# Kernel optimization log

Hardware: AMD Instinct MI355X
Metric: run time of the kernel (lower is better)

## Reference

```python
import jax, jax.numpy as jnp
import numpy as np

B, T, D = 16, 4096, 1024
UNITS = 1024


def setup_inputs() -> dict:
    key = jax.random.key(0)
    ks = jax.random.split(key, 8)
    s_in = 1.0 / np.sqrt(D)
    s_u = 1.0 / np.sqrt(UNITS)
    return {
        "hidden_state": jax.random.normal(ks[0], (B, D), jnp.float32),
        "encoder_output": jax.random.normal(ks[1], (B, T, D), jnp.float32),
        "W1": jax.random.normal(ks[2], (D, UNITS), jnp.float32) * s_in,
        "b1": jnp.zeros((UNITS,), jnp.float32),
        "W2": jax.random.normal(ks[3], (D, UNITS), jnp.float32) * s_in,
        "b2": jnp.zeros((UNITS,), jnp.float32),
        "V": jax.random.normal(ks[4], (UNITS, 1), jnp.float32) * s_u,
        "bv": jnp.zeros((1,), jnp.float32),
    }


def reference(hidden_state, encoder_output, W1, b1, W2, b2, V, bv):
    # Bahdanau additive attention: score = V(tanh(W1(h) + W2(enc)))
    h_proj = hidden_state @ W1 + b1                      # [B, U]
    e_proj = jnp.einsum("btd,du->btu", encoder_output, W2) + b2  # [B, T, U]
    feat = jnp.tanh(h_proj[:, None, :] + e_proj)          # [B, T, U]
    score = feat @ V + bv                                 # [B, T, 1]
    attention_weights = jax.nn.softmax(score, axis=1)     # [B, T, 1]
    context_vector = jnp.sum(attention_weights * encoder_output, axis=1)  # [B, D]
    return context_vector, attention_weights
```

## Files before the change

kernel.cpp:

```cpp
#include <hip/hip_runtime.h>
#include <hip/hip_bf16.h>
#include <math.h>

#define B_ 16
#define T_ 4096
#define D_ 1024
#define U_ 1024
#define M_ (B_*T_)

typedef __attribute__((ext_vector_type(8))) short short8;
typedef __attribute__((ext_vector_type(4))) short short4v;
typedef __attribute__((ext_vector_type(4))) float float4v;

static __device__ __forceinline__ short f2bf(float f) {
    unsigned u = __builtin_bit_cast(unsigned, f);
    u += 0x7FFFu + ((u >> 16) & 1u);
    return (short)(u >> 16);
}
static __device__ __forceinline__ float bf2f(short s) {
    unsigned u = ((unsigned)(unsigned short)s) << 16;
    return __builtin_bit_cast(float, u);
}
static __device__ __forceinline__ float fast_tanh(float x) {
    float c = fminf(fmaxf(2.f * x, -30.f), 30.f);
    float t = __expf(c);
    return __fdividef(t - 1.f, t + 1.f);
}

#define GLLDS(GP, LP) __builtin_amdgcn_global_load_lds( \
    (const __attribute__((address_space(1))) void*)(GP), \
    (__attribute__((address_space(3))) void*)(LP), 16, 0, 0)

__global__ void hb_kernel(const float* __restrict__ h, const float* __restrict__ W1,
                          const float* __restrict__ b1, const float* __restrict__ b2,
                          float* __restrict__ hbp) {
    int x = blockIdx.x;
    int kc = x >> 6;
    int gid = (x & 63) * 256 + threadIdx.x;
    int b = gid >> 10, u = gid & 1023;
    const float* hr = h + b * D_ + kc * 256;
    const float* w = W1 + (size_t)(kc * 256) * U_ + u;
    float s0 = 0.f, s1 = 0.f, s2 = 0.f, s3 = 0.f;
    for (int k = 0; k < 256; k += 4) {
        s0 += hr[k+0] * w[(size_t)(k+0) * U_];
        s1 += hr[k+1] * w[(size_t)(k+1) * U_];
        s2 += hr[k+2] * w[(size_t)(k+2) * U_];
        s3 += hr[k+3] * w[(size_t)(k+3) * U_];
    }
    float s = ((s0 + s1) + (s2 + s3));
    if (kc == 0) s += b1[u] + b2[u];
    hbp[kc * 16384 + gid] = s;
}

__global__ void convert_enc(const float* __restrict__ enc, short* __restrict__ encbf) {
    size_t g = (size_t)blockIdx.x * 256 + threadIdx.x;
    const float4v* p = (const float4v*)(enc + g * 16);
    float4v f0 = p[0], f1 = p[1], f2 = p[2], f3 = p[3];
    short8 a, b;
    a[0]=f2bf(f0[0]); a[1]=f2bf(f0[1]); a[2]=f2bf(f0[2]); a[3]=f2bf(f0[3]);
    a[4]=f2bf(f1[0]); a[5]=f2bf(f1[1]); a[6]=f2bf(f1[2]); a[7]=f2bf(f1[3]);
    b[0]=f2bf(f2[0]); b[1]=f2bf(f2[1]); b[2]=f2bf(f2[2]); b[3]=f2bf(f2[3]);
    b[4]=f2bf(f3[0]); b[5]=f2bf(f3[1]); b[6]=f2bf(f3[2]); b[7]=f2bf(f3[3]);
    short8* q = (short8*)(encbf + g * 16);
    q[0] = a; q[1] = b;
}

__global__ void convert_w2t(const float* __restrict__ W2, short* __restrict__ W2T) {
    __shared__ short t[64][65];
    int k0 = (blockIdx.x >> 4) * 64, u0 = (blockIdx.x & 15) * 64;
    int tx = threadIdx.x & 63, ty = threadIdx.x >> 6;
    #pragma unroll
    for (int r = 0; r < 16; ++r) {
        int kk = ty * 16 + r;
        t[kk][tx] = f2bf(W2[(size_t)(k0 + kk) * U_ + u0 + tx]);
    }
    __syncthreads();
    #pragma unroll
    for (int r = 0; r < 16; ++r) {
        int uu = ty * 16 + r;
        W2T[(size_t)(u0 + uu) * D_ + k0 + tx] = t[tx][uu];
    }
}

__global__ __launch_bounds__(256) void gemm_score_bf16(
    const short* __restrict__ Abf,
    const short* __restrict__ W2T,
    const float* __restrict__ hbp,
    const float* __restrict__ V,
    float* __restrict__ scorepart)
{
    __shared__ __align__(16) short As[128 * 32];
    __shared__ __align__(16) short Bs[128 * 32];
    __shared__ float sbuf[2][128];

    const int tid = threadIdx.x;
    const int g = blockIdx.x;
    const int c = g & 7, q = g >> 3;
    const int ntile = q & 7;
    const int mtile = (q >> 3) * 8 + c;
    const int row0 = mtile * 128, n0 = ntile * 128;
    const int bidx = row0 >> 12;

    const int lane = tid & 63, wv = tid >> 6;
    const int wm = wv >> 1, wn = wv & 1;
    const int lm = lane & 15, quad = lane >> 4;
    const int arow = tid >> 2, akq = (tid & 3) * 8;

    float4v acc[4][4] = {};

    for (int K0 = 0; K0 < D_; K0 += 32) {
        GLLDS(Abf + (size_t)(row0 + arow) * D_ + K0 + akq,       As + tid * 8);
        GLLDS(Abf + (size_t)(row0 + 64 + arow) * D_ + K0 + akq,  As + 2048 + tid * 8);
        GLLDS(W2T + (size_t)(n0 + arow) * D_ + K0 + akq,         Bs + tid * 8);
        GLLDS(W2T + (size_t)(n0 + 64 + arow) * D_ + K0 + akq,    Bs + 2048 + tid * 8);
        __syncthreads();
        short8 af[4], bfr[4];
        #pragma unroll
        for (int mi = 0; mi < 4; ++mi)
            af[mi] = *(const short8*)&As[(wm * 64 + mi * 16 + lm) * 32 + quad * 8];
        #pragma unroll
        for (int ni = 0; ni < 4; ++ni)
            bfr[ni] = *(const short8*)&Bs[(wn * 64 + ni * 16 + lm) * 32 + quad * 8];
        #pragma unroll
        for (int mi = 0; mi < 4; ++mi)
            #pragma unroll
            for (int ni = 0; ni < 4; ++ni)
                acc[mi][ni] = __builtin_amdgcn_mfma_f32_16x16x32_bf16(
                    af[mi], bfr[ni], acc[mi][ni], 0, 0, 0);
        __syncthreads();
    }

    float hbv[4], Vv[4];
    #pragma unroll
    for (int ni = 0; ni < 4; ++ni) {
        int U = n0 + wn * 64 + ni * 16 + lm;
        int o = bidx * U_ + U;
        hbv[ni] = hbp[o] + hbp[16384 + o] + hbp[32768 + o] + hbp[49152 + o];
        Vv[ni]  = V[U];
    }
    #pragma unroll
    for (int mi = 0; mi < 4; ++mi) {
        #pragma unroll
        for (int r = 0; r < 4; ++r) {
            float s = 0.f;
            #pragma unroll
            for (int ni = 0; ni < 4; ++ni)
                s += fast_tanh(acc[mi][ni][r] + hbv[ni]) * Vv[ni];
            #pragma unroll
            for (int off = 1; off < 16; off <<= 1)
                s += __shfl_xor(s, off, 64);
            if (lm == 0)
                sbuf[wn][wm * 64 + mi * 16 + quad * 4 + r] = s;
        }
    }
    __syncthreads();
    if (tid < 128)
        scorepart[(size_t)ntile * M_ + row0 + tid] = sbuf[0][tid] + sbuf[1][tid];
}

__global__ __launch_bounds__(1024) void softmax_kernel(
        const float* __restrict__ scorepart,
        const float* __restrict__ bv,
        float* __restrict__ out_attn) {
    __shared__ float sm[T_];
    __shared__ float redm[16];
    __shared__ float reds[16];
    int b = blockIdx.x, tid = threadIdx.x;
    int wv = tid >> 6;
    float bvv = bv[0];
    float lmax = -1e30f;
    #pragma unroll
    for (int i = 0; i < 4; ++i) {
        int t = tid + i * 1024;
        float s = bvv;
        #pragma unroll
        for (int p = 0; p < 8; ++p) s += scorepart[(size_t)p * M_ + b * T_ + t];
        sm[t] = s;
        lmax = fmaxf(lmax, s);
    }
    #pragma unroll
    for (int off = 1; off < 64; off <<= 1) lmax = fmaxf(lmax, __shfl_xor(lmax, off, 64));
    if ((tid & 63) == 0) redm[wv] = lmax;
    __syncthreads();
    float m = redm[0];
    #pragma unroll
    for (int j = 1; j < 16; ++j) m = fmaxf(m, redm[j]);
    float lsum = 0.f;
    #pragma unroll
    for (int i = 0; i < 4; ++i) {
        int t = tid + i * 1024;
        float e = __expf(sm[t] - m);
        sm[t] = e;
        lsum += e;
    }
    #pragma unroll
    for (int off = 1; off < 64; off <<= 1) lsum += __shfl_xor(lsum, off, 64);
    if ((tid & 63) == 0) reds[wv] = lsum;
    __syncthreads();
    float tot = 0.f;
    #pragma unroll
    for (int j = 0; j < 16; ++j) tot += reds[j];
    float rinv = 1.f / tot;
    #pragma unroll
    for (int i = 0; i < 4; ++i) {
        int t = tid + i * 1024;
        out_attn[b * T_ + t] = sm[t] * rinv;
    }
}

__global__ void ctx_part_bf(const short* __restrict__ encbf,
                            const float* __restrict__ attn,
                            float* __restrict__ part) {
    __shared__ float wsm[128];
    int x = blockIdx.x;
    int b = x & 15, tc = x >> 4;
    int tid = threadIdx.x;
    if (tid < 128) wsm[tid] = attn[b * T_ + tc * 128 + tid];
    __syncthreads();
    const short* e0 = encbf + (size_t)(b * T_ + tc * 128) * D_ + tid * 4;
    float4v acc = {};
    for (int t = 0; t < 128; ++t) {
        short4v v = *(const short4v*)(e0 + (size_t)t * D_);
        float w = wsm[t];
        acc[0] += w * bf2f(v[0]);
        acc[1] += w * bf2f(v[1]);
        acc[2] += w * bf2f(v[2]);
        acc[3] += w * bf2f(v[3]);
    }
    *(float4v*)(part + (size_t)x * 1024 + tid * 4) = acc;
}

__global__ void ctx_reduce_kernel(const float* __restrict__ part, float* __restrict__ ctx) {
    int gid = blockIdx.x * 256 + threadIdx.x;
    int b = gid >> 10, d = gid & 1023;
    float s = 0.f;
    #pragma unroll
    for (int tc = 0; tc < 32; ++tc) s += part[(size_t)(tc * 16 + b) * 1024 + d];
    ctx[gid] = s;
}

extern "C" void kernel_launch(void* const* d_in, const int* in_sizes, int n_in,
                              void* d_out, int out_size, void* d_ws, size_t ws_size,
                              hipStream_t stream) {
    const float* h   = (const float*)d_in[0];
    const float* enc = (const float*)d_in[1];
    const float* W1  = (const float*)d_in[2];
    const float* b1  = (const float*)d_in[3];
    const float* W2  = (const float*)d_in[4];
    const float* b2  = (const float*)d_in[5];
    const float* V   = (const float*)d_in[6];
    const float* bv  = (const float*)d_in[7];
    float* out = (float*)d_out;
    float* ws  = (float*)d_ws;

    float* hbp       = ws;
    float* scorepart = ws + 65536;
    float* ctxpart   = scorepart;
    short* W2T   = (short*)(ws + 65536 + 524288);
    short* encbf = (short*)((char*)W2T + (size_t)U_ * D_ * 2);

    hb_kernel<<<256, 256, 0, stream>>>(h, W1, b1, b2, hbp);
    convert_enc<<<16384, 256, 0, stream>>>(enc, encbf);
    convert_w2t<<<256, 256, 0, stream>>>(W2, W2T);
    gemm_score_bf16<<<4096, 256, 0, stream>>>(encbf, W2T, hbp, V, scorepart);
    softmax_kernel<<<16, 1024, 0, stream>>>(scorepart, bv, out + 16384);
    ctx_part_bf<<<512, 256, 0, stream>>>(encbf, out + 16384, ctxpart);
    ctx_reduce_kernel<<<64, 256, 0, stream>>>(ctxpart, out);
}
```

Before: 606.3 us.

## Rewrite score GEMM as 256x256 tile, 8-wave, double-buffered phased pipeline

The bf16 score GEMM moves from 128x128 tiles with 4 waves and a single-buffered K=32 loop to 256x256 tiles with 8 waves, K=64 steps, XOR-swizzled LDS and double buffering. Each K step is split into four MFMA phases. Global-to-LDS loads for later steps are interleaved between the phases, with explicit barriers, s_setprio and vmcnt waits. The larger tile halves the number of N-tile partial scores, so softmax now sums 4 partials instead of 8. The cost is 128KB of LDS and heavy register use, which limits occupancy, and the hand-managed waitcnt and barrier logic is fragile.

```diff
diff --git a/kernel.cpp b/kernel.cpp
--- a/kernel.cpp
+++ b/kernel.cpp
@@ -82,54 +82,136 @@
     }
 }
 
-__global__ __launch_bounds__(256) void gemm_score_bf16(
+__global__ __launch_bounds__(512, 2) void gemm_score_8ph(
     const short* __restrict__ Abf,
     const short* __restrict__ W2T,
     const float* __restrict__ hbp,
     const float* __restrict__ V,
     float* __restrict__ scorepart)
 {
-    __shared__ __align__(16) short As[128 * 32];
-    __shared__ __align__(16) short Bs[128 * 32];
-    __shared__ float sbuf[2][128];
+    __shared__ __align__(16) short lds[65536];
 
     const int tid = threadIdx.x;
     const int g = blockIdx.x;
     const int c = g & 7, q = g >> 3;
-    const int ntile = q & 7;
-    const int mtile = (q >> 3) * 8 + c;
-    const int row0 = mtile * 128, n0 = ntile * 128;
+    const int ntile = q & 3;
+    const int mtile = (q >> 2) * 8 + c;
+    const int row0 = mtile * 256, n0 = ntile * 256;
     const int bidx = row0 >> 12;
 
-    const int lane = tid & 63, wv = tid >> 6;
-    const int wm = wv >> 1, wn = wv & 1;
+    const int lane = tid & 63;
+    const int wv = tid >> 6;
+    const int wm = wv >> 2, wn = wv & 3;
     const int lm = lane & 15, quad = lane >> 4;
-    const int arow = tid >> 2, akq = (tid & 3) * 8;
-
-    float4v acc[4][4] = {};
-
-    for (int K0 = 0; K0 < D_; K0 += 32) {
-        GLLDS(Abf + (size_t)(row0 + arow) * D_ + K0 + akq,       As + tid * 8);
-        GLLDS(Abf + (size_t)(row0 + 64 + arow) * D_ + K0 + akq,  As + 2048 + tid * 8);
-        GLLDS(W2T + (size_t)(n0 + arow) * D_ + K0 + akq,         Bs + tid * 8);
-        GLLDS(W2T + (size_t)(n0 + 64 + arow) * D_ + K0 + akq,    Bs + 2048 + tid * 8);
-        __syncthreads();
-        short8 af[4], bfr[4];
+
+    const int srow = tid >> 3;
+    const int lslot = (tid & 7) ^ (srow & 7);
+    const short* aS = Abf + (size_t)(row0 + srow) * D_ + lslot * 8;
+    const short* bS = W2T + (size_t)(n0  + srow) * D_ + lslot * 8;
+    short* aD = lds + tid * 8;
+    short* bD = lds + 32768 + tid * 8;
+
+#define STG_A(kt, h, bf) do { \
+    GLLDS(aS + (size_t)((h) * 128) * D_ + (kt) * 64,      aD + (bf) * 16384 + (h) * 8192); \
+    GLLDS(aS + (size_t)((h) * 128 + 64) * D_ + (kt) * 64, aD + (bf) * 16384 + (h) * 8192 + 4096); \
+} while (0)
+#define STG_B(kt, h, bf) do { \
+    GLLDS(bS + (size_t)((h) * 128) * D_ + (kt) * 64,      bD + (bf) * 16384 + (h) * 8192); \
+    GLLDS(bS + (size_t)((h) * 128 + 64) * D_ + (kt) * 64, bD + (bf) * 16384 + (h) * 8192 + 4096); \
+} while (0)
+#define LDS_RD(off) (*(const short8*)(lds + (off)))
+#define MFMA(a, b, c) __builtin_amdgcn_mfma_f32_16x16x32_bf16((a), (b), (c), 0, 0, 0)
+
+    const int aB0 = (wm * 128 + lm) * 64 + (quad ^ (lm & 7)) * 8;
+    const int aB1 = aB0 ^ 32;
+    const int bB0 = 32768 + (wn * 64 + lm) * 64 + (quad ^ (lm & 7)) * 8;
+    const int bB1 = bB0 ^ 32;
+
+    float4v acc[8][4] = {};
+    short8 Af[4][2], Bf[4][2];
+
+    STG_A(0, 0, 0); STG_A(0, 1, 0); STG_B(0, 0, 0); STG_B(0, 1, 0);
+    STG_B(1, 0, 1); STG_A(1, 0, 1); STG_B(1, 1, 1);
+    asm volatile("s_waitcnt vmcnt(6)" ::: "memory");
+    __builtin_amdgcn_s_barrier();
+    __builtin_amdgcn_sched_barrier(0);
+
+    for (int t = 0; t < 16; ++t) {
+        const int buf = t & 1;
+        const int ab = buf * 16384;
+        #pragma unroll
+        for (int mi = 0; mi < 4; ++mi) {
+            Af[mi][0] = LDS_RD(ab + aB0 + mi * 1024);
+            Af[mi][1] = LDS_RD(ab + aB1 + mi * 1024);
+        }
+        #pragma unroll
+        for (int ni = 0; ni < 2; ++ni) {
+            Bf[ni][0] = LDS_RD(ab + bB0 + ni * 1024);
+            Bf[ni][1] = LDS_RD(ab + bB1 + ni * 1024);
+        }
+        if (t < 15) STG_A(t + 1, 1, (t + 1) & 1);
+        __builtin_amdgcn_s_barrier();
+        __builtin_amdgcn_s_setprio(1);
         #pragma unroll
         for (int mi = 0; mi < 4; ++mi)
-            af[mi] = *(const short8*)&As[(wm * 64 + mi * 16 + lm) * 32 + quad * 8];
-        #pragma unroll
-        for (int ni = 0; ni < 4; ++ni)
-            bfr[ni] = *(const short8*)&Bs[(wn * 64 + ni * 16 + lm) * 32 + quad * 8];
+            #pragma unroll
+            for (int ni = 0; ni < 2; ++ni) {
+                acc[mi][ni] = MFMA(Af[mi][0], Bf[ni][0], acc[mi][ni]);
+                acc[mi][ni] = MFMA(Af[mi][1], Bf[ni][1], acc[mi][ni]);
+            }
+        __builtin_amdgcn_s_setprio(0);
+        __builtin_amdgcn_s_barrier();
+        #pragma unroll
+        for (int ni = 0; ni < 2; ++ni) {
+            Bf[2 + ni][0] = LDS_RD(ab + bB0 + (2 + ni) * 1024);
+            Bf[2 + ni][1] = LDS_RD(ab + bB1 + (2 + ni) * 1024);
+        }
+        __builtin_amdgcn_s_barrier();
+        __builtin_amdgcn_s_setprio(1);
         #pragma unroll
         for (int mi = 0; mi < 4; ++mi)
             #pragma unroll
-            for (int ni = 0; ni < 4; ++ni)
-                acc[mi][ni] = __builtin_amdgcn_mfma_f32_16x16x32_bf16(
-                    af[mi], bfr[ni], acc[mi][ni], 0, 0, 0);
-        __syncthreads();
-    }
-
+            for (int ni = 0; ni < 2; ++ni) {
+                acc[mi][2 + ni] = MFMA(Af[mi][0], Bf[2 + ni][0], acc[mi][2 + ni]);
+                acc[mi][2 + ni] = MFMA(Af[mi][1], Bf[2 + ni][1], acc[mi][2 + ni]);
+            }
+        __builtin_amdgcn_s_setprio(0);
+        __builtin_amdgcn_s_barrier();
+        #pragma unroll
+        for (int mi = 0; mi < 4; ++mi) {
+            Af[mi][0] = LDS_RD(ab + aB0 + 4096 + mi * 1024);
+            Af[mi][1] = LDS_RD(ab + aB1 + 4096 + mi * 1024);
+        }
+        if (t < 14) STG_B(t + 2, 0, buf);
+        __builtin_amdgcn_s_barrier();
+        __builtin_amdgcn_s_setprio(1);
+        #pragma unroll
+        for (int mi = 0; mi < 4; ++mi)
+            #pragma unroll
+            for (int ni = 0; ni < 2; ++ni) {
+                acc[4 + mi][ni] = MFMA(Af[mi][0], Bf[ni][0], acc[4 + mi][ni]);
+                acc[4 + mi][ni] = MFMA(Af[mi][1], Bf[ni][1], acc[4 + mi][ni]);
+            }
+        __builtin_amdgcn_s_setprio(0);
+        __builtin_amdgcn_s_barrier();
+        if (t < 14) { STG_A(t + 2, 0, buf); STG_B(t + 2, 1, buf); }
+        __builtin_amdgcn_s_barrier();
+        __builtin_amdgcn_s_setprio(1);
+        #pragma unroll
+        for (int mi = 0; mi < 4; ++mi)
+            #pragma unroll
+            for (int ni = 0; ni < 2; ++ni) {
+                acc[4 + mi][2 + ni] = MFMA(Af[mi][0], Bf[2 + ni][0], acc[4 + mi][2 + ni]);
+                acc[4 + mi][2 + ni] = MFMA(Af[mi][1], Bf[2 + ni][1], acc[4 + mi][2 + ni]);
+            }
+        __builtin_amdgcn_s_setprio(0);
+        if (t < 14)      { asm volatile("s_waitcnt vmcnt(6)" ::: "memory"); }
+        else if (t == 14){ asm volatile("s_waitcnt vmcnt(0)" ::: "memory"); }
+        __builtin_amdgcn_s_barrier();
+        __builtin_amdgcn_sched_barrier(0);
+    }
+
+    float* sbuf = (float*)lds;
     float hbv[4], Vv[4];
     #pragma unroll
     for (int ni = 0; ni < 4; ++ni) {
@@ -139,7 +221,7 @@
         Vv[ni]  = V[U];
     }
     #pragma unroll
-    for (int mi = 0; mi < 4; ++mi) {
+    for (int mi = 0; mi < 8; ++mi) {
         #pragma unroll
         for (int r = 0; r < 4; ++r) {
             float s = 0.f;
@@ -150,12 +232,13 @@
             for (int off = 1; off < 16; off <<= 1)
                 s += __shfl_xor(s, off, 64);
             if (lm == 0)
-                sbuf[wn][wm * 64 + mi * 16 + quad * 4 + r] = s;
-        }
-    }
-    __syncthreads();
-    if (tid < 128)
-        scorepart[(size_t)ntile * M_ + row0 + tid] = sbuf[0][tid] + sbuf[1][tid];
+                sbuf[wn * 256 + wm * 128 + mi * 16 + quad * 4 + r] = s;
+        }
+    }
+    __syncthreads();
+    if (tid < 256)
+        scorepart[(size_t)ntile * M_ + row0 + tid] =
+            sbuf[tid] + sbuf[256 + tid] + sbuf[512 + tid] + sbuf[768 + tid];
 }
 
 __global__ __launch_bounds__(1024) void softmax_kernel(
@@ -174,7 +257,7 @@
         int t = tid + i * 1024;
         float s = bvv;
         #pragma unroll
-        for (int p = 0; p < 8; ++p) s += scorepart[(size_t)p * M_ + b * T_ + t];
+        for (int p = 0; p < 4; ++p) s += scorepart[(size_t)p * M_ + b * T_ + t];
         sm[t] = s;
         lmax = fmaxf(lmax, s);
     }
@@ -262,7 +345,7 @@
     hb_kernel<<<256, 256, 0, stream>>>(h, W1, b1, b2, hbp);
     convert_enc<<<16384, 256, 0, stream>>>(enc, encbf);
     convert_w2t<<<256, 256, 0, stream>>>(W2, W2T);
-    gemm_score_bf16<<<4096, 256, 0, stream>>>(encbf, W2T, hbp, V, scorepart);
+    gemm_score_8ph<<<1024, 512, 0, stream>>>(encbf, W2T, hbp, V, scorepart);
     softmax_kernel<<<16, 1024, 0, stream>>>(scorepart, bv, out + 16384);
     ctx_part_bf<<<512, 256, 0, stream>>>(encbf, out + 16384, ctxpart);
     ctx_reduce_kernel<<<64, 256, 0, stream>>>(ctxpart, out);
```

Result: faster. 575.7 us (-5.1%).
